# Performance work log

Hardware: AMD Instinct MI355X
Metric: run time of the kernel (lower is better)

## Reference

```python
import jax, jax.numpy as jnp
import numpy as np

NEG = -9.0e15
D = 768


def _init_params(key, d):
    ks = jax.random.split(key, 12)
    s = 0.02
    p = {}
    p['Wa'] = jax.random.normal(ks[0], (d, 1), jnp.float32) * s
    p['ba'] = jnp.zeros((1,), jnp.float32)
    for i, name in enumerate(['qs', 'ks', 'qc', 'kc', 'qr', 'kr']):
        p['W' + name] = jax.random.normal(ks[1 + i], (d, d), jnp.float32) * s
        p['b' + name] = jnp.zeros((d,), jnp.float32)
    p['Wf1'] = jax.random.normal(ks[8], (3 * d, d), jnp.float32) * s
    p['bf1'] = jnp.zeros((d,), jnp.float32)
    p['Wf2'] = jax.random.normal(ks[9], (d, d), jnp.float32) * s
    p['bf2'] = jnp.zeros((d,), jnp.float32)
    p['gamma'] = jnp.ones((d,), jnp.float32)
    p['beta'] = jnp.zeros((d,), jnp.float32)
    return p


def setup_inputs() -> dict:
    key = jax.random.key(0)
    k1, k2, k3 = jax.random.split(key, 3)
    B, L = 8, 1024
    inp = {
        'x': jax.random.normal(k1, (B, L, D), jnp.float32),
        'x_ids': jax.random.randint(k2, (B, L), 0, 1000, jnp.int64 if jax.config.read('jax_enable_x64') else jnp.int32).astype(jnp.int32),
        'pad_idx': 0,
    }
    inp.update(_init_params(k3, D))
    return inp


def _forward(x, x_ids, pad_idx, Wa, ba, Wqs, bqs, Wks, bks, Wqc, bqc, Wkc, bkc,
             Wqr, bqr, Wkr, bkr, Wf1, bf1, Wf2, bf2, gamma, beta):
    B, L, d = x.shape
    valid = x_ids != pad_idx                             # [B,L]
    valid_len = valid.sum(axis=1)
    sep_pos = jnp.clip(valid_len // 2, 1, max(1, L - 2))  # [B]
    pos = jnp.arange(L)[None, :]                          # [1,L]
    false_mask = (pos < sep_pos[:, None]) & valid         # [B,L]
    option_mask = (pos > sep_pos[:, None]) & valid        # [B,L]

    # anomaly gate over false segment
    a_logits = (x @ Wa + ba)[..., 0]                      # [B,L]
    a_logits = jnp.where(false_mask, a_logits, NEG)
    gate = jax.nn.softmax(a_logits, axis=1) * false_mask.astype(x.dtype)
    gate = gate / jnp.clip(gate.sum(axis=1, keepdims=True), 1e-8)

    scale = 1.0 / jnp.sqrt(jnp.asarray(d, x.dtype))
    q_sup, k_sup = x @ Wqs + bqs, x @ Wks + bks
    q_con, k_con = x @ Wqc + bqc, x @ Wkc + bkc
    q_rep, k_rep = x @ Wqr + bqr, x @ Wkr + bkr

    sup_s = jnp.einsum('bld,bmd->blm', q_sup, k_sup) * scale
    con_s = jnp.einsum('bld,bmd->blm', q_con, k_con) * scale
    rep_s = jnp.einsum('bld,bmd->blm', q_rep, k_rep) * scale

    pair_mask = false_mask[:, :, None] & option_mask[:, None, :]  # [B,L,L]
    sup_attn = jax.nn.softmax(jnp.where(pair_mask, sup_s, NEG), axis=-1)
    rep_attn = jax.nn.softmax(jnp.where(pair_mask, rep_s + jnp.tanh(con_s), NEG), axis=-1)

    rep_vec = jnp.einsum('blm,bmd->bld', rep_attn, x)
    sup_vec = jnp.einsum('blm,bmd->bld', sup_attn, x)

    anomaly_false = jnp.einsum('bl,bld->bd', gate, x)
    w_rep = jnp.einsum('bl,bld->bd', gate, rep_vec)
    w_sup = jnp.einsum('bl,bld->bd', gate, sup_vec)

    fused = jnp.concatenate([anomaly_false, w_rep, w_sup], axis=-1)
    fused = jnp.maximum(fused @ Wf1 + bf1, 0.0) @ Wf2 + bf2  # dropout = eval identity

    mu = fused.mean(axis=-1, keepdims=True)
    var = ((fused - mu) ** 2).mean(axis=-1, keepdims=True)
    fused = (fused - mu) / jnp.sqrt(var + 1e-5) * gamma + beta
    return fused


def reference(x, x_ids, pad_idx, Wa, ba, Wqs, bqs, Wks, bks, Wqc, bqc, Wkc, bkc,
              Wqr, bqr, Wkr, bkr, Wf1, bf1, Wf2, bf2, gamma, beta):
    return _forward(x, x_ids, pad_idx, Wa, ba, Wqs, bqs, Wks, bks, Wqc, bqc,
                    Wkc, bkc, Wqr, bqr, Wkr, bkr, Wf1, bf1, Wf2, bf2, gamma, beta)
```

## Files before the change

### kernel.cpp

```cpp
#include <hip/hip_runtime.h>
#include <math.h>

#define L 1024
#define NB 8
#define D 768
#define NEGV (-9.0e15f)
#define SCALE 0.036084391824351615f

typedef unsigned short u16;
typedef __attribute__((ext_vector_type(8))) short short8;
typedef __attribute__((ext_vector_type(4))) float float4v;
#define MFMA_BF16 __builtin_amdgcn_mfma_f32_16x16x32_bf16

__device__ __forceinline__ float b2f(u16 u) {
    union { unsigned int i; float f; } v; v.i = ((unsigned int)u) << 16; return v.f;
}
__device__ __forceinline__ u16 f2b(float f) {
    union { float fv; unsigned int i; } v; v.fv = f;
    unsigned int x = v.i;
    x += 0x7fffu + ((x >> 16) & 1u);
    return (u16)(x >> 16);
}
__device__ __forceinline__ float unpk(unsigned int w, int h) {
    return b2f((u16)(h ? (w >> 16) : (w & 0xffffu)));
}

template<int F32>
__device__ __forceinline__ float4 ld4(const void* p, size_t idx) {
    if (F32) return *(const float4*)((const float*)p + idx);
    ushort4 v = *(const ushort4*)((const u16*)p + idx);
    return make_float4(b2f(v.x), b2f(v.y), b2f(v.z), b2f(v.w));
}
template<int F32>
__device__ __forceinline__ float ld1(const void* p, size_t idx) {
    if (F32) return ((const float*)p)[idx];
    return b2f(((const u16*)p)[idx]);
}
__device__ __forceinline__ int ldid(const int* p, size_t idx, int is64) {
    return is64 ? p[idx * 2] : p[idx];
}

__device__ __forceinline__ void detect2(const void* x, const void* ids, int* sh) {
    int tid = threadIdx.x;
    if (tid < 64) {
        u16 u = ((const u16*)x)[tid * 2];
        int e = (u >> 7) & 0xFF;
        unsigned long long balf = __ballot(e >= 100 && e <= 140);
        int v = ((const int*)ids)[tid * 2 + 1];
        unsigned long long bali = __ballot(v != 0);
        if (tid == 0) {
            sh[0] = (__popcll(balf) < 32) ? 1 : 0;
            sh[1] = (bali == 0ULL) ? 1 : 0;
        }
    }
    __syncthreads();
}

#define WS_FLAG  ((size_t)0)
#define WS_SEP   ((size_t)64)
#define WS_C0    ((size_t)128)
#define WS_Z0    ((size_t)192)
#define WS_W1    ((size_t)9472)
#define WS_GATE  ((size_t)18752)
#define WS_CSUP  ((size_t)51520)
#define WS_CREP  ((size_t)84288)
#define WS_AF    ((size_t)117056)
#define WS_WREP  ((size_t)141632)
#define WS_WSUP  ((size_t)166208)
#define WS_HACC  ((size_t)190784)
#define WS_ALOG  ((size_t)215360)
#define WS_T     ((size_t)248128)
#define WS_OACC  ((size_t)303104)
#define WS_XB    ((size_t)524288)
#define WS_Z     ((size_t)13107200)
#define WS_WB    ((size_t)31981568)
#define WS_M     ((size_t)40370176)

struct PP { const void* W[6]; const void* b[6]; };

template<int F32> __device__ void kbias_body(const void* W, const void* vec,
        float* out, float* vs, int xi) {
    int tid = threadIdx.x;
    for (int i = tid; i < D; i += 256) vs[i] = ld1<F32>(vec, i);
    __syncthreads();
    int row = xi * 64 + (tid >> 2);
    int sub = tid & 3;
    float acc = 0.f;
    for (int i = 0; i < 48; ++i) {
        int k = i * 16 + sub * 4;
        float4 wv = ld4<F32>(W, (size_t)row * D + k);
        acc += wv.x * vs[k] + wv.y * vs[k + 1] + wv.z * vs[k + 2] + wv.w * vs[k + 3];
    }
    acc += __shfl_xor(acc, 1);
    acc += __shfl_xor(acc, 2);
    if (sub == 0) out[row] = acc;
}
template<int F32> __device__ void kc0_body(const void* bq, const void* bk,
        float* c0, float* red) {
    int tid = threadIdx.x;
    float s = 0.f;
    for (int i = tid; i < D; i += 256) s += ld1<F32>(bq, i) * ld1<F32>(bk, i);
    red[tid] = s; __syncthreads();
    for (int st = 128; st > 0; st >>= 1) { if (tid < st) red[tid] += red[tid + st]; __syncthreads(); }
    if (tid == 0) c0[0] = red[0];
}

template<int F32> __device__ void kx_body(const void* x, const void* Wa,
        const void* ba, u16* xb, float* alog, float* ws2) {
    int tid = threadIdx.x;
    for (int i = tid; i < D; i += 256) ws2[i] = ld1<F32>(Wa, i);
    __syncthreads();
    int row = blockIdx.x * 32 + (tid >> 3);
    int sub = tid & 7;
    float a0 = 0.f;
    for (int i = 0; i < 24; ++i) {
        int k = i * 32 + sub * 4;
        float4 xv = ld4<F32>(x, (size_t)row * D + k);
        ushort4 o;
        o.x = f2b(xv.x); o.y = f2b(xv.y); o.z = f2b(xv.z); o.w = f2b(xv.w);
        *(ushort4*)(xb + (size_t)row * D + k) = o;
        a0 += xv.x * ws2[k] + xv.y * ws2[k + 1] + xv.z * ws2[k + 2] + xv.w * ws2[k + 3];
    }
    #pragma unroll
    for (int d = 1; d < 8; d <<= 1) a0 += __shfl_xor(a0, d);
    if (sub == 0) alog[row] = a0 + ld1<F32>(ba, 0);
}
__global__ __launch_bounds__(256) void kx(const void* x, const int* ids, PP pp,
        const void* Wa, const void* ba, u16* xb, u16* Wb, float* alog,
        float* z0, float* w1, float* c0f) {
    __shared__ float sf[2 * D];
    __shared__ int fsh[2];
    detect2(x, ids, fsh);
    int F32 = fsh[0];
    int bid = blockIdx.x;
    if (bid < 256) {
        if (F32) kx_body<1>(x, Wa, ba, xb, alog, sf);
        else     kx_body<0>(x, Wa, ba, xb, alog, sf);
        return;
    }
    if (bid < 1984) {
        int t = (bid - 256) / 288, inner = (bid - 256) % 288;
        const void* src = pp.W[t];
        u16* dst = Wb + (size_t)t * D * D;
        size_t base = ((size_t)inner * 256 + threadIdx.x) * 8;
        if (F32) {
            float4 a = *(const float4*)((const float*)src + base);
            float4 b = *(const float4*)((const float*)src + base + 4);
            uint4 o; u16* po = (u16*)&o;
            po[0] = f2b(a.x); po[1] = f2b(a.y); po[2] = f2b(a.z); po[3] = f2b(a.w);
            po[4] = f2b(b.x); po[5] = f2b(b.y); po[6] = f2b(b.z); po[7] = f2b(b.w);
            *(uint4*)(dst + base) = o;
        } else {
            *(uint4*)(dst + base) = *(const uint4*)((const u16*)src + base);
        }
        return;
    }
    int i = bid - 1984;
    int y = i / 12, xi = i % 12;
    float* vs = sf;
    float* red = sf + D;
    if (y == 4) {
        if (xi != 0) return;
        if (F32) kc0_body<1>(pp.b[2], pp.b[3], c0f, red);
        else     kc0_body<0>(pp.b[2], pp.b[3], c0f, red);
        return;
    }
    const void* W; const void* vec; float* out;
    if (y < 3) { W = pp.W[2 * y + 1]; vec = pp.b[2 * y]; out = z0 + y * D; }
    else       { W = pp.W[2];         vec = pp.b[3];     out = w1; }
    if (F32) kbias_body<1>(W, vec, out, vs, xi);
    else     kbias_body<0>(W, vec, out, vs, xi);
}

__device__ __forceinline__ void stage128_async(const u16* __restrict__ G, size_t ld,
        int r0, int k0, u16* S, int tid) {
    int rowa = tid >> 2;
    int koa = ((tid & 3) ^ (rowa & 3)) << 3;
    int wave = tid >> 6;
    const u16* g1 = &G[(size_t)(r0 + rowa) * ld + k0 + koa];
    const u16* g2 = &G[(size_t)(r0 + rowa + 64) * ld + k0 + koa];
    __builtin_amdgcn_global_load_lds((__attribute__((address_space(1))) void*)(u16*)g1,
        (__attribute__((address_space(3))) void*)(S + wave * 512), 16, 0, 0);
    __builtin_amdgcn_global_load_lds((__attribute__((address_space(1))) void*)(u16*)g2,
        (__attribute__((address_space(3))) void*)(S + 2048 + wave * 512), 16, 0, 0);
}
__device__ __forceinline__ void stage64_async(const u16* __restrict__ G, size_t ld,
        int r0, int k0, u16* S, int tid) {
    int rowa = tid >> 2;
    int koa = ((tid & 3) ^ (rowa & 3)) << 3;
    int wave = tid >> 6;
    const u16* g = &G[(size_t)(r0 + rowa) * ld + k0 + koa];
    __builtin_amdgcn_global_load_lds((__attribute__((address_space(1))) void*)(u16*)g,
        (__attribute__((address_space(3))) void*)(S + wave * 512), 16, 0, 0);
}

__device__ __forceinline__ void gemm64_cnt(const u16* __restrict__ A, size_t lda, int r0,
        const u16* __restrict__ B, size_t ldb, int c0,
        u16* As, u16* Bs, float4v acc[2][4]) {
    int tid = threadIdx.x;
    int lane = tid & 63, wave = tid >> 6;
    int wm = (wave >> 1) << 5, wn = (wave & 1) << 6;
    int quad = lane >> 4, lrow = lane & 15;
    int sq = ((quad ^ (lrow & 3)) << 3);
    #pragma unroll
    for (int i = 0; i < 2; ++i)
        #pragma unroll
        for (int j = 0; j < 4; ++j) acc[i][j] = (float4v){0.f, 0.f, 0.f, 0.f};
    stage64_async(A, lda, r0, 0, As, tid);
    stage64_async(A, lda, r0, 32, As + 2048, tid);
    stage128_async(B, ldb, c0, 0, Bs, tid);
    stage128_async(B, ldb, c0, 32, Bs + 4096, tid);
    stage64_async(A, lda, r0, 64, As + 4096, tid);
    stage64_async(A, lda, r0, 96, As + 6144, tid);
    stage128_async(B, ldb, c0, 64, Bs + 8192, tid);
    stage128_async(B, ldb, c0, 96, Bs + 12288, tid);
    #pragma unroll 1
    for (int t = 0; t < 12; ++t) {
        int cur = t & 1;
        if (t != 11) asm volatile("s_waitcnt vmcnt(6)" ::: "memory");
        else         asm volatile("s_waitcnt vmcnt(0)" ::: "memory");
        __builtin_amdgcn_s_barrier();
        const u16* Ab = As + cur * 4096;
        const u16* Bb = Bs + cur * 8192;
        short8 fa[2][2], fb[2][4];
        #pragma unroll
        for (int p = 0; p < 2; ++p) {
            #pragma unroll
            for (int i = 0; i < 2; ++i)
                fa[p][i] = *(const short8*)&Ab[p * 2048 + (wm + i * 16 + lrow) * 32 + sq];
            #pragma unroll
            for (int j = 0; j < 4; ++j)
                fb[p][j] = *(const short8*)&Bb[p * 4096 + (wn + j * 16 + lrow) * 32 + sq];
        }
        asm volatile("s_waitcnt lgkmcnt(0)" ::: "memory");
        __builtin_amdgcn_sched_barrier(0);
        __builtin_amdgcn_s_barrier();
        if (t < 10) {
            int k0 = (t + 2) << 6;
            u16* Ad = As + cur * 4096;
            u16* Bd = Bs + cur * 8192;
            stage64_async(A, lda, r0, k0, Ad, tid);
            stage64_async(A, lda, r0, k0 + 32, Ad + 2048, tid);
            stage128_async(B, ldb, c0, k0, Bd, tid);
            stage128_async(B, ldb, c0, k0 + 32, Bd + 4096, tid);
        }
        #pragma unroll
        for (int p = 0; p < 2; ++p)
            #pragma unroll
            for (int i = 0; i < 2; ++i)
                #pragma unroll
                for (int j = 0; j < 4; ++j)
                    acc[i][j] = MFMA_BF16(fa[p][i], fb[p][j], acc[i][j], 0, 0, 0);
    }
}

__device__ __forceinline__ void gemm128_cnt(const u16* __restrict__ A, size_t lda, int r0,
        const u16* __restrict__ B, size_t ldb, int c0,
        u16* As, u16* Bs, float4v acc[4][4]) {
    int tid = threadIdx.x;
    int lane = tid & 63, wave = tid >> 6;
    int wm = (wave >> 1) << 6, wn = (wave & 1) << 6;
    int quad = lane >> 4, lrow = lane & 15;
    int sq = ((quad ^ (lrow & 3)) << 3);
    #pragma unroll
    for (int i = 0; i < 4; ++i)
        #pragma unroll
        for (int j = 0; j < 4; ++j) acc[i][j] = (float4v){0.f, 0.f, 0.f, 0.f};
    stage128_async(A, lda, r0, 0, As, tid);
    stage128_async(A, lda, r0, 32, As + 4096, tid);
    stage128_async(B, ldb, c0, 0, Bs, tid);
    stage128_async(B, ldb, c0, 32, Bs + 4096, tid);
    stage128_async(A, lda, r0, 64, As + 8192, tid);
    stage128_async(A, lda, r0, 96, As + 12288, tid);
    stage128_async(B, ldb, c0, 64, Bs + 8192, tid);
    stage128_async(B, ldb, c0, 96, Bs + 12288, tid);
    #pragma unroll 1
    for (int t = 0; t < 12; ++t) {
        int cur = t & 1;
        if (t != 11) asm volatile("s_waitcnt vmcnt(8)" ::: "memory");
        else         asm volatile("s_waitcnt vmcnt(0)" ::: "memory");
        __builtin_amdgcn_s_barrier();
        const u16* Ab = As + cur * 8192;
        const u16* Bb = Bs + cur * 8192;
        short8 fa[2][4], fb[2][4];
        #pragma unroll
        for (int p = 0; p < 2; ++p) {
            #pragma unroll
            for (int i = 0; i < 4; ++i)
                fa[p][i] = *(const short8*)&Ab[p * 4096 + (wm + i * 16 + lrow) * 32 + sq];
            #pragma unroll
            for (int j = 0; j < 4; ++j)
                fb[p][j] = *(const short8*)&Bb[p * 4096 + (wn + j * 16 + lrow) * 32 + sq];
        }
        asm volatile("s_waitcnt lgkmcnt(0)" ::: "memory");
        __builtin_amdgcn_sched_barrier(0);
        __builtin_amdgcn_s_barrier();
        if (t < 10) {
            int k0 = (t + 2) << 6;
            u16* Ad = As + cur * 8192;
            u16* Bd = Bs + cur * 8192;
            stage128_async(A, lda, r0, k0, Ad, tid);
            stage128_async(A, lda, r0, k0 + 32, Ad + 4096, tid);
            stage128_async(B, ldb, c0, k0, Bd, tid);
            stage128_async(B, ldb, c0, k0 + 32, Bd + 4096, tid);
        }
        #pragma unroll
        for (int p = 0; p < 2; ++p)
            #pragma unroll
            for (int i = 0; i < 4; ++i)
                #pragma unroll
                for (int j = 0; j < 4; ++j)
                    acc[i][j] = MFMA_BF16(fa[p][i], fb[p][j], acc[i][j], 0, 0, 0);
    }
}

__global__ __launch_bounds__(256) void kB(const void* x, const int* __restrict__ ids,
        const int* __restrict__ padp, const float* __restrict__ alog,
        float* __restrict__ gate, int* __restrict__ sepArr,
        float* __restrict__ af, float* __restrict__ wrep, float* __restrict__ wsup,
        float* __restrict__ hacc, float* __restrict__ oacc,
        float* __restrict__ csup, float* __restrict__ crep,
        const u16* __restrict__ xb, const float* __restrict__ w1,
        const float* __restrict__ c0f, float* __restrict__ tbuf,
        const u16* __restrict__ Wb, u16* __restrict__ Mt) {
    __shared__ __align__(16) u16 SMEM[24576];
    int bid = blockIdx.x;
    int tid = threadIdx.x;
    if (bid >= 8 && bid < 224) {
        int i = bid - 8;
        int p = i / 72, j = i % 72;
        int r0 = (j / 6) * 64, c0m = (j % 6) * 128;
        u16* As = SMEM;
        u16* Bs = SMEM + 8192;
        float4v acc[2][4];
        gemm64_cnt(Wb + (size_t)(2 * p + 1) * D * D, D, r0,
                   Wb + (size_t)(2 * p) * D * D, D, c0m, As, Bs, acc);
        int lane = tid & 63, wave = tid >> 6;
        int wm = (wave >> 1) << 5, wn = (wave & 1) << 6;
        int quad = lane >> 4, lrow = lane & 15;
        u16* out = Mt + (size_t)p * D * D;
        #pragma unroll
        for (int ii = 0; ii < 2; ++ii)
            #pragma unroll
            for (int jj = 0; jj < 4; ++jj) {
                int brow = r0 + wm + ii * 16 + quad * 4;
                int col = c0m + wn + jj * 16 + lrow;
                #pragma unroll
                for (int r = 0; r < 4; ++r)
                    out[(size_t)(brow + r) * D + col] = f2b(acc[ii][jj][r]);
            }
        return;
    }
    if (bid >= 224) {
        int i = bid - 224;
        int b = i >> 2, q = i & 3;
        float* w1s = (float*)SMEM;
        for (int j = tid; j < D; j += 256) w1s[j] = w1[j];
        __syncthreads();
        float c0v = c0f[0];
        int sub = tid & 15;
        int rowi = tid >> 4;
        for (int pass = 0; pass < 8; ++pass) {
            int l = q * 128 + pass * 16 + rowi;
            const u16* xr = xb + ((size_t)b * L + l) * D;
            float a = 0.f;
            #pragma unroll
            for (int i2 = 0; i2 < 6; ++i2) {
                int k = i2 * 128 + sub * 8;
                short8 v = *(const short8*)&xr[k];
                #pragma unroll
                for (int e = 0; e < 8; ++e) a += b2f((u16)v[e]) * w1s[k + e];
            }
            #pragma unroll
            for (int d2 = 1; d2 < 16; d2 <<= 1) a += __shfl_xor(a, d2);
            if (sub == 0) tbuf[b * 512 + l] = a + c0v;
        }
        return;
    }
    float* red = (float*)SMEM;
    int*   ish = (int*)(red + 256);
    detect2(x, ids, ish);
    int is64 = ish[1];
    int b = bid;
    int pad = padp[0];
    int cnt = 0;
    for (int l = tid; l < L; l += 256) cnt += (ldid(ids, (size_t)b * L + l, is64) != pad) ? 1 : 0;
    red[tid] = (float)cnt; __syncthreads();
    for (int s = 128; s > 0; s >>= 1) { if (tid < s) red[tid] += red[tid + s]; __syncthreads(); }
    if (tid == 0) {
        int vl = (int)red[0];
        int sep = vl / 2; if (sep < 1) sep = 1; if (sep > L - 2) sep = L - 2;
        ish[2] = sep; sepArr[b] = sep;
    }
    __syncthreads();
    int sep = ish[2];
    float lv[4]; int lidx[4];
    float mx = -3.4e38f;
    for (int u = 0; u < 4; ++u) {
        int l = tid + u * 256; lidx[u] = l;
        bool fm = (l < sep) && (ldid(ids, (size_t)b * L + l, is64) != pad);
        float v = fm ? alog[b * L + l] : NEGV;
        lv[u] = v; mx = fmaxf(mx, v);
    }
    red[tid] = mx; __syncthreads();
    for (int s = 128; s > 0; s >>= 1) { if (tid < s) red[tid] = fmaxf(red[tid], red[tid + s]); __syncthreads(); }
    mx = red[0]; __syncthreads();
    float se = 0.f;
    for (int u = 0; u < 4; ++u) { lv[u] = expf(lv[u] - mx); se += lv[u]; }
    red[tid] = se; __syncthreads();
    for (int s = 128; s > 0; s >>= 1) { if (tid < s) red[tid] += red[tid + s]; __syncthreads(); }
    float den = fmaxf(red[0], 1e-30f); __syncthreads();
    float gs = 0.f; float gv[4];
    for (int u = 0; u < 4; ++u) {
        int l = lidx[u];
        bool fm = (l < sep) && (ldid(ids, (size_t)b * L + l, is64) != pad);
        float p = lv[u] / den;
        gv[u] = fm ? p : 0.f;
        gs += gv[u];
    }
    red[tid] = gs; __syncthreads();
    for (int s = 128; s > 0; s >>= 1) { if (tid < s) red[tid] += red[tid + s]; __syncthreads(); }
    gs = red[0];
    float inv = 1.f / fmaxf(gs, 1e-8f);
    for (int u = 0; u < 4; ++u) gate[b * L + lidx[u]] = gv[u] * inv;
    for (int l = tid; l < L; l += 256) { csup[b * L + l] = 0.f; crep[b * L + l] = 0.f; }
    for (int i = tid; i < D; i += 256) {
        af[b * D + i] = 0.f; wrep[b * D + i] = 0.f; wsup[b * D + i] = 0.f;
        hacc[b * D + i] = 0.f; oacc[b * D + i] = 0.f;
    }
}

__global__ __launch_bounds__(256) void kZ_mfma(const u16* __restrict__ xb,
        const u16* __restrict__ Mt, const float* __restrict__ z0,
        u16* __restrict__ Zbuf, const int* __restrict__ sepArr) {
    __shared__ __align__(16) u16 As[16384];
    __shared__ __align__(16) u16 Bs[16384];
    int z = blockIdx.z;
    int p = z >> 3, b = z & 7;
    int sep = sepArr[b];
    int r0 = blockIdx.y * 128;
    if (r0 >= sep) return;
    int c0 = blockIdx.x * 128;
    float4v acc[4][4];
    gemm128_cnt(xb + (size_t)b * L * D, D, r0,
                Mt + (size_t)p * D * D, D, c0, As, Bs, acc);
    int lane = threadIdx.x & 63, wave = threadIdx.x >> 6;
    int wm = (wave >> 1) << 6, wn = (wave & 1) << 6;
    int quad = lane >> 4, lrow = lane & 15;
    const float* z0p = z0 + p * D;
    u16* out = Zbuf + ((size_t)p * NB + b) * 512 * D;
    #pragma unroll
    for (int i = 0; i < 4; ++i)
        #pragma unroll
        for (int j = 0; j < 4; ++j) {
            int brow = r0 + wm + i * 16 + quad * 4;
            int col = c0 + wn + j * 16 + lrow;
            float zb = z0p[col];
            #pragma unroll
            for (int r = 0; r < 4; ++r)
                out[(size_t)(brow + r) * D + col] = f2b(acc[i][j][r] + zb);
        }
}

__global__ __launch_bounds__(512) void kS2(const u16* __restrict__ Zbuf,
        const u16* __restrict__ xb, const float* __restrict__ tcbuf,
        const int* __restrict__ sepArr, const int* __restrict__ ids,
        const int* __restrict__ padp, const float* __restrict__ gate,
        float* __restrict__ csup, float* __restrict__ crep) {
    __shared__ float redmx[2][8][16];
    __shared__ float redsm[2][8][16];
    __shared__ int ish[1];
    int bid = blockIdx.x;
    int b = bid & 7;
    int l0 = (bid >> 3) * 16;
    int sep = sepArr[b];
    int tid = threadIdx.x, lane = tid & 63, wave = tid >> 6;
    int lrow = lane & 15, quad = lane >> 4;
    if (tid < 64) {
        int v = ((const int*)ids)[tid * 2 + 1];
        unsigned long long bali = __ballot(v != 0);
        if (tid == 0) ish[0] = (bali == 0ULL) ? 1 : 0;
    }
    __syncthreads();
    if (l0 >= sep) return;
    int is64 = ish[0];
    int pad = padp[0];
    int msta = ((sep + 1) >> 7) << 7;
    int nchunk = (L - msta) >> 7;
    size_t aoff = (size_t)(l0 + lrow) * D + quad * 8;
    const u16* pA0 = Zbuf + (size_t)b * 512 * D + aoff;
    const u16* pA1 = Zbuf + ((size_t)NB + b) * 512 * D + aoff;
    const u16* pA2 = Zbuf + ((size_t)2 * NB + b) * 512 * D + aoff;
    const u16* X  = xb + (size_t)b * L * D;
    float tcv[4], gr[4];
    #pragma unroll
    for (int r = 0; r < 4; ++r) {
        tcv[r] = tcbuf[b * 512 + l0 + quad * 4 + r];
        gr[r]  = gate[b * L + l0 + quad * 4 + r];
    }
    unsigned int pS[8][2], pC[8][2];
    #pragma unroll
    for (int g = 0; g < 2; ++g) {
      if (g * 4 < nchunk) {
        const u16 *pB0_, *pB1_, *pB2_, *pB3_;
        {
            int m00 = msta + (g * 4 + 0) * 128; if (m00 > L - 128) m00 = L - 128;
            int m01 = msta + (g * 4 + 1) * 128; if (m01 > L - 128) m01 = L - 128;
            int m02 = msta + (g * 4 + 2) * 128; if (m02 > L - 128) m02 = L - 128;
            int m03 = msta + (g * 4 + 3) * 128; if (m03 > L - 128) m03 = L - 128;
            pB0_ = X + (size_t)(m00 + wave * 16 + lrow) * D + quad * 8;
            pB1_ = X + (size_t)(m01 + wave * 16 + lrow) * D + quad * 8;
            pB2_ = X + (size_t)(m02 + wave * 16 + lrow) * D + quad * 8;
            pB3_ = X + (size_t)(m03 + wave * 16 + lrow) * D + quad * 8;
        }
        float4v acc[3][4];
        #pragma unroll
        for (int m = 0; m < 3; ++m)
            #pragma unroll
            for (int cc = 0; cc < 4; ++cc) acc[m][cc] = (float4v){0.f, 0.f, 0.f, 0.f};
        short8 A0a, A1a, A2a, B0a, B1a, B2a, B3a;
        short8 A0b, A1b, A2b, B0b, B1b, B2b, B3b;
        short8 A0c, A1c, A2c, B0c, B1c, B2c, B3c;
#define LDSTEP(SUF, S) do { int ko_ = (S) * 32; \
        A0##SUF = *(const short8*)(pA0 + ko_); \
        A1##SUF = *(const short8*)(pA1 + ko_); \
        A2##SUF = *(const short8*)(pA2 + ko_); \
        B0##SUF = *(const short8*)(pB0_ + ko_); \
        B1##SUF = *(const short8*)(pB1_ + ko_); \
        B2##SUF = *(const short8*)(pB2_ + ko_); \
        B3##SUF = *(const short8*)(pB3_ + ko_); } while (0)
#define CPSTEP(SUF) do { \
        acc[0][0] = MFMA_BF16(A0##SUF, B0##SUF, acc[0][0], 0, 0, 0); \
        acc[1][0] = MFMA_BF16(A1##SUF, B0##SUF, acc[1][0], 0, 0, 0); \
        acc[2][0] = MFMA_BF16(A2##SUF, B0##SUF, acc[2][0], 0, 0, 0); \
        acc[0][1] = MFMA_BF16(A0##SUF, B1##SUF, acc[0][1], 0, 0, 0); \
        acc[1][1] = MFMA_BF16(A1##SUF, B1##SUF, acc[1][1], 0, 0, 0); \
        acc[2][1] = MFMA_BF16(A2##SUF, B1##SUF, acc[2][1], 0, 0, 0); \
        acc[0][2] = MFMA_BF16(A0##SUF, B2##SUF, acc[0][2], 0, 0, 0); \
        acc[1][2] = MFMA_BF16(A1##SUF, B2##SUF, acc[1][2], 0, 0, 0); \
        acc[2][2] = MFMA_BF16(A2##SUF, B2##SUF, acc[2][2], 0, 0, 0); \
        acc[0][3] = MFMA_BF16(A0##SUF, B3##SUF, acc[0][3], 0, 0, 0); \
        acc[1][3] = MFMA_BF16(A1##SUF, B3##SUF, acc[1][3], 0, 0, 0); \
        acc[2][3] = MFMA_BF16(A2##SUF, B3##SUF, acc[2][3], 0, 0, 0); } while (0)
        LDSTEP(a, 0); LDSTEP(b, 1); LDSTEP(c, 2);
        #pragma unroll
        for (int it = 0; it < 8; ++it) {
            CPSTEP(a); if (it * 3 + 3 < 24) LDSTEP(a, it * 3 + 3);
            CPSTEP(b); if (it * 3 + 4 < 24) LDSTEP(b, it * 3 + 4);
            CPSTEP(c); if (it * 3 + 5 < 24) LDSTEP(c, it * 3 + 5);
        }
#undef LDSTEP
#undef CPSTEP
        #pragma unroll
        for (int cc = 0; cc < 4; ++cc) {
            int c = g * 4 + cc;
            if (c < nchunk) {
                int m = msta + c * 128 + wave * 16 + lrow;
                bool ok = (m > sep) && (ldid(ids, (size_t)b * L + m, is64) != pad);
                float vs[4], vc[4];
                #pragma unroll
                for (int r = 0; r < 4; ++r) {
                    vs[r] = ok ? acc[0][cc][r] * SCALE : NEGV;
                    vc[r] = ok ? (acc[2][cc][r] * SCALE
                                  + tanhf((acc[1][cc][r] + tcv[r]) * SCALE)) : NEGV;
                }
                pS[c][0] = (unsigned)f2b(vs[0]) | ((unsigned)f2b(vs[1]) << 16);
                pS[c][1] = (unsigned)f2b(vs[2]) | ((unsigned)f2b(vs[3]) << 16);
                pC[c][0] = (unsigned)f2b(vc[0]) | ((unsigned)f2b(vc[1]) << 16);
                pC[c][1] = (unsigned)f2b(vc[2]) | ((unsigned)f2b(vc[3]) << 16);
            }
        }
      }
    }
    float mxs[4], mxc[4];
    #pragma unroll
    for (int r = 0; r < 4; ++r) { mxs[r] = -3.4e38f; mxc[r] = -3.4e38f; }
    #pragma unroll
    for (int c = 0; c < 8; ++c) if (c < nchunk)
        #pragma unroll
        for (int r = 0; r < 4; ++r) {
            mxs[r] = fmaxf(mxs[r], unpk(pS[c][r >> 1], r & 1));
            mxc[r] = fmaxf(mxc[r], unpk(pC[c][r >> 1], r & 1));
        }
    #pragma unroll
    for (int d = 1; d < 16; d <<= 1)
        #pragma unroll
        for (int r = 0; r < 4; ++r) {
            mxs[r] = fmaxf(mxs[r], __shfl_xor(mxs[r], d));
            mxc[r] = fmaxf(mxc[r], __shfl_xor(mxc[r], d));
        }
    if (lrow == 0)
        #pragma unroll
        for (int r = 0; r < 4; ++r) {
            redmx[0][wave][quad * 4 + r] = mxs[r];
            redmx[1][wave][quad * 4 + r] = mxc[r];
        }
    __syncthreads();
    #pragma unroll
    for (int r = 0; r < 4; ++r) {
        int rr = quad * 4 + r;
        float m0 = redmx[0][0][rr], m1 = redmx[1][0][rr];
        #pragma unroll
        for (int w = 1; w < 8; ++w) {
            m0 = fmaxf(m0, redmx[0][w][rr]);
            m1 = fmaxf(m1, redmx[1][w][rr]);
        }
        mxs[r] = m0; mxc[r] = m1;
    }
    float sms[4], smc[4];
    #pragma unroll
    for (int r = 0; r < 4; ++r) { sms[r] = 0.f; smc[r] = 0.f; }
    #pragma unroll
    for (int c = 0; c < 8; ++c) if (c < nchunk)
        #pragma unroll
        for (int r = 0; r < 4; ++r) {
            sms[r] += expf(unpk(pS[c][r >> 1], r & 1) - mxs[r]);
            smc[r] += expf(unpk(pC[c][r >> 1], r & 1) - mxc[r]);
        }
    #pragma unroll
    for (int d = 1; d < 16; d <<= 1)
        #pragma unroll
        for (int r = 0; r < 4; ++r) {
            sms[r] += __shfl_xor(sms[r], d);
            smc[r] += __shfl_xor(smc[r], d);
        }
    if (lrow == 0)
        #pragma unroll
        for (int r = 0; r < 4; ++r) {
            redsm[0][wave][quad * 4 + r] = sms[r];
            redsm[1][wave][quad * 4 + r] = smc[r];
        }
    __syncthreads();
    float wgs[4], wgc[4];
    #pragma unroll
    for (int r = 0; r < 4; ++r) {
        int rr = quad * 4 + r;
        float d0 = redsm[0][0][rr], d1 = redsm[1][0][rr];
        #pragma unroll
        for (int w = 1; w < 8; ++w) {
            d0 += redsm[0][w][rr];
            d1 += redsm[1][w][rr];
        }
        wgs[r] = gr[r] / fmaxf(d0, 1e-30f);
        wgc[r] = gr[r] / fmaxf(d1, 1e-30f);
    }
    #pragma unroll
    for (int c = 0; c < 8; ++c) if (c < nchunk) {
        float as = 0.f, ar = 0.f;
        #pragma unroll
        for (int r = 0; r < 4; ++r) {
            as += wgs[r] * expf(unpk(pS[c][r >> 1], r & 1) - mxs[r]);
            ar += wgc[r] * expf(unpk(pC[c][r >> 1], r & 1) - mxc[r]);
        }
        as += __shfl_xor(as, 16); as += __shfl_xor(as, 32);
        ar += __shfl_xor(ar, 16); ar += __shfl_xor(ar, 32);
        if (quad == 0) {
            int m = msta + c * 128 + wave * 16 + lrow;
            atomicAdd(&csup[b * L + m], as);
            atomicAdd(&crep[b * L + m], ar);
        }
    }
}

__global__ __launch_bounds__(256) void k3(const u16* __restrict__ xb,
        const float* __restrict__ gate, const float* __restrict__ csup,
        const float* __restrict__ crep, float* __restrict__ af,
        float* __restrict__ wrep, float* __restrict__ wsup) {
    int b = blockIdx.y, c = blockIdx.x;
    int tid = threadIdx.x;
    float a0 = 0.f, a1 = 0.f, a2 = 0.f;
    float r0 = 0.f, r1 = 0.f, r2 = 0.f;
    float q0 = 0.f, q1 = 0.f, q2 = 0.f;
    for (int mm = 0; mm < 16; ++mm) {
        int m = c * 16 + mm;
        float wg = gate[b * L + m], wr = crep[b * L + m], wq = csup[b * L + m];
        if (wg == 0.f && wr == 0.f && wq == 0.f) continue;
        size_t base = ((size_t)b * L + m) * D;
        float x0 = b2f(xb[base + tid]);
        float x1 = b2f(xb[base + tid + 256]);
        float x2 = b2f(xb[base + tid + 512]);
        a0 += wg * x0; a1 += wg * x1; a2 += wg * x2;
        r0 += wr * x0; r1 += wr * x1; r2 += wr * x2;
        q0 += wq * x0; q1 += wq * x1; q2 += wq * x2;
    }
    atomicAdd(&af[b * D + tid], a0); atomicAdd(&af[b * D + tid + 256], a1); atomicAdd(&af[b * D + tid + 512], a2);
    atomicAdd(&wrep[b * D + tid], r0); atomicAdd(&wrep[b * D + tid + 256], r1); atomicAdd(&wrep[b * D + tid + 512], r2);
    atomicAdd(&wsup[b * D + tid], q0); atomicAdd(&wsup[b * D + tid + 256], q1); atomicAdd(&wsup[b * D + tid + 512], q2);
}

template<int F32> __device__ void kh1_body(const float* af, const float* wrep,
        const float* wsup, const void* Wf1, float* hacc, float* fs) {
    int tid = threadIdx.x;
    int c0 = blockIdx.x * 128, k0 = blockIdx.y * 144;
    for (int e = tid; e < 8 * 144; e += 256) {
        int b = e / 144, kk = e - b * 144;
        int k = k0 + kk;
        float v = (k < D) ? af[b * D + k] : (k < 2 * D) ? wrep[b * D + k - D]
                                                        : wsup[b * D + k - 2 * D];
        fs[b * 144 + kk] = v;
    }
    __syncthreads();
    int col = c0 + (tid & 127);
    int kg = tid >> 7;
    float acc[NB];
    #pragma unroll
    for (int b = 0; b < NB; ++b) acc[b] = 0.f;
    #pragma unroll 4
    for (int r = 0; r < 72; ++r) {
        int kk = kg * 72 + r;
        float w = ld1<F32>(Wf1, (size_t)(k0 + kk) * D + col);
        #pragma unroll
        for (int b = 0; b < NB; ++b) acc[b] += fs[b * 144 + kk] * w;
    }
    #pragma unroll
    for (int b = 0; b < NB; ++b) atomicAdd(&hacc[b * D + col], acc[b]);
}
__global__ __launch_bounds__(256) void kh1(const void* x, const int* ids,
        const float* af, const float* wrep,
        const float* wsup, const void* Wf1, float* hacc) {
    __shared__ float fs[8 * 144];
    __shared__ int fsh[2];
    detect2(x, ids, fsh);
    if (fsh[0]) kh1_body<1>(af, wrep, wsup, Wf1, hacc, fs);
    else        kh1_body<0>(af, wrep, wsup, Wf1, hacc, fs);
}

template<int F32> __device__ void kh2_body(const float* hacc, const void* bf1,
        const void* Wf2, float* oacc, float* hsl) {
    int tid = threadIdx.x;
    int c0 = blockIdx.x * 128, k0 = blockIdx.y * 96;
    for (int e = tid; e < 8 * 96; e += 256) {
        int b = e / 96, kk = e - b * 96;
        int k = k0 + kk;
        hsl[b * 96 + kk] = fmaxf(hacc[b * D + k] + ld1<F32>(bf1, k), 0.f);
    }
    __syncthreads();
    int col = c0 + (tid & 127);
    int kg = tid >> 7;
    float acc[NB];
    #pragma unroll
    for (int b = 0; b < NB; ++b) acc[b] = 0.f;
    #pragma unroll 4
    for (int r = 0; r < 48; ++r) {
        int kk = kg * 48 + r;
        float w = ld1<F32>(Wf2, (size_t)(k0 + kk) * D + col);
        #pragma unroll
        for (int b = 0; b < NB; ++b) acc[b] += hsl[b * 96 + kk] * w;
    }
    #pragma unroll
    for (int b = 0; b < NB; ++b) atomicAdd(&oacc[b * D + col], acc[b]);
}
__global__ __launch_bounds__(256) void kh2(const void* x, const int* ids,
        const float* hacc, const void* bf1,
        const void* Wf2, float* oacc) {
    __shared__ float hsl[8 * 96];
    __shared__ int fsh[2];
    detect2(x, ids, fsh);
    if (fsh[0]) kh2_body<1>(hacc, bf1, Wf2, oacc, hsl);
    else        kh2_body<0>(hacc, bf1, Wf2, oacc, hsl);
}

template<int F32> __device__ void kln_body(const float* oacc, const void* bf2,
        const void* gamma, const void* beta, void* out, float* red) {
    int b = blockIdx.x, tid = threadIdx.x;
    float o[3];
    #pragma unroll
    for (int u = 0; u < 3; ++u) {
        int i = tid + u * 256;
        o[u] = oacc[b * D + i] + ld1<F32>(bf2, i);
    }
    red[tid] = o[0] + o[1] + o[2]; __syncthreads();
    for (int s = 128; s > 0; s >>= 1) { if (tid < s) red[tid] += red[tid + s]; __syncthreads(); }
    float mu = red[0] / (float)D; __syncthreads();
    float vs = 0.f;
    #pragma unroll
    for (int u = 0; u < 3; ++u) vs += (o[u] - mu) * (o[u] - mu);
    red[tid] = vs; __syncthreads();
    for (int s = 128; s > 0; s >>= 1) { if (tid < s) red[tid] += red[tid + s]; __syncthreads(); }
    float var = red[0] / (float)D;
    float rstd = 1.0f / sqrtf(var + 1e-5f);
    #pragma unroll
    for (int u = 0; u < 3; ++u) {
        int i = tid + u * 256;
        float v = (o[u] - mu) * rstd * ld1<F32>(gamma, i) + ld1<F32>(beta, i);
        if (F32) ((float*)out)[b * D + i] = v;
        else     ((u16*)out)[b * D + i] = f2b(v);
    }
}
__global__ __launch_bounds__(256) void kln(const void* x, const int* ids,
        const float* oacc, const void* bf2,
        const void* gamma, const void* beta, void* out) {
    __shared__ float red[256];
    __shared__ int fsh[2];
    detect2(x, ids, fsh);
    if (fsh[0]) kln_body<1>(oacc, bf2, gamma, beta, out, red);
    else        kln_body<0>(oacc, bf2, gamma, beta, out, red);
}

extern "C" void kernel_launch(void* const* d_in, const int* in_sizes, int n_in,
                              void* d_out, int out_size, void* d_ws, size_t ws_size,
                              hipStream_t stream) {
    const void* x    = d_in[0];
    const int* ids   = (const int*)d_in[1];
    const int* padp  = (const int*)d_in[2];
    const void* Wa   = d_in[3];
    const void* ba   = d_in[4];
    PP pp;
    pp.W[0] = d_in[5];  pp.b[0] = d_in[6];
    pp.W[1] = d_in[7];  pp.b[1] = d_in[8];
    pp.W[2] = d_in[9];  pp.b[2] = d_in[10];
    pp.W[3] = d_in[11]; pp.b[3] = d_in[12];
    pp.W[4] = d_in[13]; pp.b[4] = d_in[14];
    pp.W[5] = d_in[15]; pp.b[5] = d_in[16];
    const void* Wf1 = d_in[17]; const void* bf1 = d_in[18];
    const void* Wf2 = d_in[19]; const void* bf2 = d_in[20];
    const void* gamma = d_in[21]; const void* beta = d_in[22];

    char* ws = (char*)d_ws;
    int*   sepArr = (int*)(ws + WS_SEP);
    float* c0   = (float*)(ws + WS_C0);
    float* z0   = (float*)(ws + WS_Z0);
    float* w1   = (float*)(ws + WS_W1);
    float* gate = (float*)(ws + WS_GATE);
    float* csup = (float*)(ws + WS_CSUP);
    float* crep = (float*)(ws + WS_CREP);
    float* af   = (float*)(ws + WS_AF);
    float* wrep = (float*)(ws + WS_WREP);
    float* wsup = (float*)(ws + WS_WSUP);
    float* hacc = (float*)(ws + WS_HACC);
    float* oacc = (float*)(ws + WS_OACC);
    float* alog = (float*)(ws + WS_ALOG);
    float* tbuf = (float*)(ws + WS_T);
    u16* xb   = (u16*)(ws + WS_XB);
    u16* Zbuf = (u16*)(ws + WS_Z);
    u16* Wb   = (u16*)(ws + WS_WB);
    u16* Mt   = (u16*)(ws + WS_M);

    kx<<<dim3(2044), dim3(256), 0, stream>>>(x, ids, pp, Wa, ba, xb, Wb, alog, z0, w1, c0);
    kB<<<dim3(256), dim3(256), 0, stream>>>(x, ids, padp, alog, gate, sepArr,
                                            af, wrep, wsup, hacc, oacc, csup, crep,
                                            xb, w1, c0, tbuf, Wb, Mt);
    kZ_mfma<<<dim3(6, 4, 24), dim3(256), 0, stream>>>(xb, Mt, z0, Zbuf, sepArr);
    kS2<<<dim3(256), dim3(512), 0, stream>>>(Zbuf, xb, tbuf, sepArr, ids, padp,
                                             gate, csup, crep);
    k3<<<dim3(64, NB), dim3(256), 0, stream>>>(xb, gate, csup, crep, af, wrep, wsup);
    kh1<<<dim3(6, 16), dim3(256), 0, stream>>>(x, ids, af, wrep, wsup, Wf1, hacc);
    kh2<<<dim3(6, 8), dim3(256), 0, stream>>>(x, ids, hacc, bf1, Wf2, oacc);
    kln<<<dim3(NB), dim3(256), 0, stream>>>(x, ids, oacc, bf2, gamma, beta, d_out);
}
```

Baseline: 261.8 us.

## Stage A1/A2 query tiles in swizzled LDS and hand-schedule global loads with inline asm

Two of the three query-side operand tiles (A1, A2) of the score kernel are now loaded once per block into XOR-swizzled shared memory instead of being re-read from global memory by every wave. The remaining global loads (A0 and the four key tiles) are issued through inline asm global_load_dwordx4 with immediate offsets. A fully unrolled schedule with explicit s_waitcnt vmcnt and sched_barrier keeps three K-steps of loads in flight. This is meant to cut redundant global traffic and VGPR pressure, at the cost of 48KB of LDS per block, which may lower occupancy. The manual waitcnt scheme depends on the compiler not inserting other vector memory ops, which is fragile.

```diff
diff --git a/kernel.cpp b/kernel.cpp
--- a/kernel.cpp
+++ b/kernel.cpp
@@ -467,6 +467,7 @@
         const int* __restrict__ sepArr, const int* __restrict__ ids,
         const int* __restrict__ padp, const float* __restrict__ gate,
         float* __restrict__ csup, float* __restrict__ crep) {
+    __shared__ __align__(16) u16 Alds[24576];
     __shared__ float redmx[2][8][16];
     __shared__ float redsm[2][8][16];
     __shared__ int ish[1];
@@ -487,17 +488,28 @@
     int pad = padp[0];
     int msta = ((sep + 1) >> 7) << 7;
     int nchunk = (L - msta) >> 7;
-    size_t aoff = (size_t)(l0 + lrow) * D + quad * 8;
-    const u16* pA0 = Zbuf + (size_t)b * 512 * D + aoff;
-    const u16* pA1 = Zbuf + ((size_t)NB + b) * 512 * D + aoff;
-    const u16* pA2 = Zbuf + ((size_t)2 * NB + b) * 512 * D + aoff;
+    const u16* A0 = Zbuf + (size_t)b * 512 * D;
+    const u16* A1 = Zbuf + ((size_t)NB + b) * 512 * D;
+    const u16* A2 = Zbuf + ((size_t)2 * NB + b) * 512 * D;
     const u16* X  = xb + (size_t)b * L * D;
+    #pragma unroll
+    for (int i = 0; i < 6; ++i) {
+        int s = tid + i * 512;
+        int m = s / 1536, rem = s - m * 1536;
+        int r = rem / 96, c = rem - r * 96;
+        const u16* src = (m == 0 ? A1 : A2) + (size_t)(l0 + r) * D + c * 8;
+        *(short8*)&Alds[(((m * 16 + r) * 96) + (c ^ (r & 7))) * 8] = *(const short8*)src;
+    }
+    __syncthreads();
     float tcv[4], gr[4];
     #pragma unroll
     for (int r = 0; r < 4; ++r) {
         tcv[r] = tcbuf[b * 512 + l0 + quad * 4 + r];
         gr[r]  = gate[b * L + l0 + quad * 4 + r];
     }
+    int xr = lrow & 7;
+    int arow0 = lrow * 768;
+    const u16* pA0_ = A0 + (size_t)(l0 + lrow) * D + quad * 8;
     unsigned int pS[8][2], pC[8][2];
     #pragma unroll
     for (int g = 0; g < 2; ++g) {
@@ -518,38 +530,67 @@
         for (int m = 0; m < 3; ++m)
             #pragma unroll
             for (int cc = 0; cc < 4; ++cc) acc[m][cc] = (float4v){0.f, 0.f, 0.f, 0.f};
-        short8 A0a, A1a, A2a, B0a, B1a, B2a, B3a;
-        short8 A0b, A1b, A2b, B0b, B1b, B2b, B3b;
-        short8 A0c, A1c, A2c, B0c, B1c, B2c, B3c;
-#define LDSTEP(SUF, S) do { int ko_ = (S) * 32; \
-        A0##SUF = *(const short8*)(pA0 + ko_); \
-        A1##SUF = *(const short8*)(pA1 + ko_); \
-        A2##SUF = *(const short8*)(pA2 + ko_); \
-        B0##SUF = *(const short8*)(pB0_ + ko_); \
-        B1##SUF = *(const short8*)(pB1_ + ko_); \
-        B2##SUF = *(const short8*)(pB2_ + ko_); \
-        B3##SUF = *(const short8*)(pB3_ + ko_); } while (0)
+        short8 fA1, fA2;
+        short8 A0a, B0a, B1a, B2a, B3a;
+        short8 A0b, B0b, B1b, B2b, B3b;
+        short8 A0c, B0c, B1c, B2c, B3c;
+#define GL_(dst, base, imm) asm volatile("global_load_dwordx4 %0, %1, off offset:" #imm : "=v"(dst) : "v"(base))
+#define GL(dst, base, imm) GL_(dst, base, imm)
+#define LDG5(SUF, IMM) do { \
+        GL(A0##SUF, pA0_, IMM); \
+        GL(B0##SUF, pB0_, IMM); GL(B1##SUF, pB1_, IMM); \
+        GL(B2##SUF, pB2_, IMM); GL(B3##SUF, pB3_, IMM); } while (0)
+#define LDA(S) do { int sw = (((4 * (S) + quad) ^ xr) << 3); \
+        fA1 = *(const short8*)&Alds[arow0 + sw]; \
+        fA2 = *(const short8*)&Alds[12288 + arow0 + sw]; } while (0)
+#define WAITN_(N) do { asm volatile("s_waitcnt vmcnt(" #N ")"); \
+        __builtin_amdgcn_sched_barrier(0); } while (0)
+#define WAITN(N) WAITN_(N)
 #define CPSTEP(SUF) do { \
         acc[0][0] = MFMA_BF16(A0##SUF, B0##SUF, acc[0][0], 0, 0, 0); \
-        acc[1][0] = MFMA_BF16(A1##SUF, B0##SUF, acc[1][0], 0, 0, 0); \
-        acc[2][0] = MFMA_BF16(A2##SUF, B0##SUF, acc[2][0], 0, 0, 0); \
+        acc[1][0] = MFMA_BF16(fA1, B0##SUF, acc[1][0], 0, 0, 0); \
+        acc[2][0] = MFMA_BF16(fA2, B0##SUF, acc[2][0], 0, 0, 0); \
         acc[0][1] = MFMA_BF16(A0##SUF, B1##SUF, acc[0][1], 0, 0, 0); \
-        acc[1][1] = MFMA_BF16(A1##SUF, B1##SUF, acc[1][1], 0, 0, 0); \
-        acc[2][1] = MFMA_BF16(A2##SUF, B1##SUF, acc[2][1], 0, 0, 0); \
+        acc[1][1] = MFMA_BF16(fA1, B1##SUF, acc[1][1], 0, 0, 0); \
+        acc[2][1] = MFMA_BF16(fA2, B1##SUF, acc[2][1], 0, 0, 0); \
         acc[0][2] = MFMA_BF16(A0##SUF, B2##SUF, acc[0][2], 0, 0, 0); \
-        acc[1][2] = MFMA_BF16(A1##SUF, B2##SUF, acc[1][2], 0, 0, 0); \
-        acc[2][2] = MFMA_BF16(A2##SUF, B2##SUF, acc[2][2], 0, 0, 0); \
+        acc[1][2] = MFMA_BF16(fA1, B2##SUF, acc[1][2], 0, 0, 0); \
+        acc[2][2] = MFMA_BF16(fA2, B2##SUF, acc[2][2], 0, 0, 0); \
         acc[0][3] = MFMA_BF16(A0##SUF, B3##SUF, acc[0][3], 0, 0, 0); \
-        acc[1][3] = MFMA_BF16(A1##SUF, B3##SUF, acc[1][3], 0, 0, 0); \
-        acc[2][3] = MFMA_BF16(A2##SUF, B3##SUF, acc[2][3], 0, 0, 0); } while (0)
-        LDSTEP(a, 0); LDSTEP(b, 1); LDSTEP(c, 2);
-        #pragma unroll
-        for (int it = 0; it < 8; ++it) {
-            CPSTEP(a); if (it * 3 + 3 < 24) LDSTEP(a, it * 3 + 3);
-            CPSTEP(b); if (it * 3 + 4 < 24) LDSTEP(b, it * 3 + 4);
-            CPSTEP(c); if (it * 3 + 5 < 24) LDSTEP(c, it * 3 + 5);
-        }
-#undef LDSTEP
+        acc[1][3] = MFMA_BF16(fA1, B3##SUF, acc[1][3], 0, 0, 0); \
+        acc[2][3] = MFMA_BF16(fA2, B3##SUF, acc[2][3], 0, 0, 0); } while (0)
+        WAITN(0);
+        LDG5(a, 0); LDG5(b, 64); LDG5(c, 128);
+        LDA(0);  WAITN(10); CPSTEP(a); LDG5(a, 192);
+        LDA(1);  WAITN(10); CPSTEP(b); LDG5(b, 256);
+        LDA(2);  WAITN(10); CPSTEP(c); LDG5(c, 320);
+        LDA(3);  WAITN(10); CPSTEP(a); LDG5(a, 384);
+        LDA(4);  WAITN(10); CPSTEP(b); LDG5(b, 448);
+        LDA(5);  WAITN(10); CPSTEP(c); LDG5(c, 512);
+        LDA(6);  WAITN(10); CPSTEP(a); LDG5(a, 576);
+        LDA(7);  WAITN(10); CPSTEP(b); LDG5(b, 640);
+        LDA(8);  WAITN(10); CPSTEP(c); LDG5(c, 704);
+        LDA(9);  WAITN(10); CPSTEP(a); LDG5(a, 768);
+        LDA(10); WAITN(10); CPSTEP(b); LDG5(b, 832);
+        LDA(11); WAITN(10); CPSTEP(c); LDG5(c, 896);
+        LDA(12); WAITN(10); CPSTEP(a); LDG5(a, 960);
+        LDA(13); WAITN(10); CPSTEP(b); LDG5(b, 1024);
+        LDA(14); WAITN(10); CPSTEP(c); LDG5(c, 1088);
+        LDA(15); WAITN(10); CPSTEP(a); LDG5(a, 1152);
+        LDA(16); WAITN(10); CPSTEP(b); LDG5(b, 1216);
+        LDA(17); WAITN(10); CPSTEP(c); LDG5(c, 1280);
+        LDA(18); WAITN(10); CPSTEP(a); LDG5(a, 1344);
+        LDA(19); WAITN(10); CPSTEP(b); LDG5(b, 1408);
+        LDA(20); WAITN(10); CPSTEP(c); LDG5(c, 1472);
+        LDA(21); WAITN(10); CPSTEP(a);
+        LDA(22); WAITN(5);  CPSTEP(b);
+        LDA(23); WAITN(0);  CPSTEP(c);
+#undef GL_
+#undef GL
+#undef LDG5
+#undef LDA
+#undef WAITN_
+#undef WAITN
 #undef CPSTEP
         #pragma unroll
         for (int cc = 0; cc < 4; ++cc) {
```

Result: faster. 252.4 us (median of 2 runs) (-3.6%).
